# Performance work log

Measured on AMD Instinct MI355X. Metric: run time of the kernel, lower is better.

## Reference

```python
import jax, jax.numpy as jnp
import numpy as np

LN_EPS = 1e-5

def layer_norm(x, g, b):
    m = x.mean(-1, keepdims=True)
    v = ((x - m) ** 2).mean(-1, keepdims=True)
    return (x - m) / jnp.sqrt(v + LN_EPS) * g + b

def gat_conv(x, src, dst, W, att_src, att_dst, bias, heads, out_ch, concat):
    # PyG GATConv (eval mode, self-loops already included in src/dst).
    N = x.shape[0]
    h = (x @ W).reshape(N, heads, out_ch)                 # [N,H,C]
    a_src = (h * att_src).sum(-1)                          # [N,H]
    a_dst = (h * att_dst).sum(-1)                          # [N,H]
    e = jax.nn.leaky_relu(a_src[src] + a_dst[dst], 0.2)   # [E,H]
    emax = jax.ops.segment_max(e, dst, num_segments=N)    # [N,H]
    ee = jnp.exp(e - emax[dst])
    denom = jax.ops.segment_sum(ee, dst, num_segments=N)  # [N,H]
    alpha = ee / (denom[dst] + 1e-16)                      # [E,H]
    out = jax.ops.segment_sum(alpha[:, :, None] * h[src], dst, num_segments=N)  # [N,H,C]
    out = out.reshape(N, heads * out_ch) if concat else out.mean(axis=1)
    return out + bias

def setup_inputs() -> dict:
    key = jax.random.key(0)
    ks = jax.random.split(key, 32)
    N, G, E = 50000, 405, 300000
    RH, GH, H = 256, 256, 4
    def w(k, shape, fan_in):
        return jax.random.normal(k, shape, dtype=jnp.float32) * (1.0 / np.sqrt(fan_in))
    d = {}
    d["x"] = jax.random.normal(ks[0], (N, G), dtype=jnp.float32)
    d["edge_index"] = jax.random.randint(ks[1], (2, E), 0, N, dtype=jnp.int64)
    # JointEncoder
    d["enc_w1"] = w(ks[2], (G, RH), G); d["enc_b1"] = jnp.zeros(RH)
    d["ln1_g"] = jnp.ones(RH); d["ln1_b"] = jnp.zeros(RH)
    d["enc_w2"] = w(ks[3], (RH, RH), RH); d["enc_b2"] = jnp.zeros(RH)
    d["ln2_g"] = jnp.ones(RH); d["ln2_b"] = jnp.zeros(RH)
    d["w1"] = w(ks[4], (RH, H * GH), RH)
    d["att_src1"] = w(ks[5], (H, GH), GH); d["att_dst1"] = w(ks[6], (H, GH), GH)
    d["bias1"] = jnp.zeros(H * GH)
    d["res1_w"] = w(ks[7], (RH, H * GH), RH); d["res1_b"] = jnp.zeros(H * GH)
    d["w2"] = w(ks[8], (H * GH, 2 * 96), H * GH)
    d["att_src2"] = w(ks[9], (2, 96), 96); d["att_dst2"] = w(ks[10], (2, 96), 96)
    d["bias2"] = jnp.zeros(2 * 96)
    d["res2_w"] = w(ks[11], (H * GH, 2 * 96), H * GH); d["res2_b"] = jnp.zeros(2 * 96)
    d["w3"] = w(ks[12], (192, 128), 192)
    d["att_src3"] = w(ks[13], (1, 128), 128); d["att_dst3"] = w(ks[14], (1, 128), 128)
    d["bias3"] = jnp.zeros(128)
    d["res3_w"] = w(ks[15], (192, 128), 192); d["res3_b"] = jnp.zeros(128)
    # MLP head
    d["mlp_w1"] = w(ks[16], (128, 64), 128); d["mlp_b1"] = jnp.zeros(64)
    d["mlp_w2"] = w(ks[17], (64, 2), 64); d["mlp_b2"] = jnp.zeros(2)
    return d

def reference(x, edge_index, enc_w1, enc_b1, ln1_g, ln1_b, enc_w2, enc_b2, ln2_g, ln2_b,
              w1, att_src1, att_dst1, bias1, res1_w, res1_b,
              w2, att_src2, att_dst2, bias2, res2_w, res2_b,
              w3, att_src3, att_dst3, bias3, res3_w, res3_b,
              mlp_w1, mlp_b1, mlp_w2, mlp_b2):
    N = x.shape[0]
    loop = jnp.arange(N, dtype=edge_index.dtype)
    src = jnp.concatenate([edge_index[0], loop])
    dst = jnp.concatenate([edge_index[1], loop])
    # JointEncoder (eval: dropout is identity)
    h = jax.nn.relu(layer_norm(x @ enc_w1 + enc_b1, ln1_g, ln1_b))
    h = jax.nn.relu(layer_norm(h @ enc_w2 + enc_b2, ln2_g, ln2_b))
    # Block 1
    idn = h
    h = jax.nn.elu(gat_conv(h, src, dst, w1, att_src1, att_dst1, bias1, 4, 256, True))
    h = h + (idn @ res1_w + res1_b)
    # Block 2
    idn = h
    h = jax.nn.elu(gat_conv(h, src, dst, w2, att_src2, att_dst2, bias2, 2, 96, True))
    h = h + (idn @ res2_w + res2_b)
    # Block 3
    idn = h
    h = jax.nn.elu(gat_conv(h, src, dst, w3, att_src3, att_dst3, bias3, 1, 128, False))
    h = h + (idn @ res3_w + res3_b)
    # MLP head
    out = jax.nn.relu(h @ mlp_w1 + mlp_b1) @ mlp_w2 + mlp_b2
    return out
```

## Files before the change

kernel.cpp:

```cpp
#include <hip/hip_runtime.h>
#include <cstddef>

#define LN_EPS 1e-5f

typedef __bf16 bf16x8 __attribute__((ext_vector_type(8)));
typedef float  f32x4  __attribute__((ext_vector_type(4)));

typedef __attribute__((address_space(3))) unsigned int lds_u32;
typedef __attribute__((address_space(1))) unsigned int glb_u32;

__device__ __forceinline__ void gl2lds16(const void* g, void* l) {
    __builtin_amdgcn_global_load_lds((const glb_u32*)g, (lds_u32*)l, 16, 0, 0);
}

__device__ __forceinline__ float b2f(ushort h) {
    return __uint_as_float(((unsigned)h) << 16);
}
__device__ __forceinline__ ushort f2b(float f) {
    unsigned u = __float_as_uint(f);
    return (ushort)((u + 0x7fffu + ((u >> 16) & 1u)) >> 16);
}
__device__ __forceinline__ unsigned pack2(float lo, float hi) {
    return (unsigned)f2b(lo) | ((unsigned)f2b(hi) << 16);
}
__device__ __forceinline__ uint2 pack4(const f32x4 v) {
    return make_uint2(pack2(v[0], v[1]), pack2(v[2], v[3]));
}

__device__ __forceinline__ void xcd_map(int& bx, int& by) {
    int NX = gridDim.x, MBr = gridDim.y;
    int L = blockIdx.y * NX + blockIdx.x;
    int G = NX * 8;
    int g = L / G;
    if (g * 8 + 8 <= MBr) {
        int r = L - g * G;
        by = g * 8 + (r & 7);
        bx = r >> 3;
    } else {
        by = L / NX;
        bx = L - by * NX;
    }
}

__device__ __forceinline__ float wave_reduce_sum(float v) {
    #pragma unroll
    for (int off = 32; off > 0; off >>= 1) v += __shfl_down(v, off, 64);
    return v;
}
__device__ __forceinline__ float wave_allreduce_max(float v) {
    #pragma unroll
    for (int off = 32; off > 0; off >>= 1) v = fmaxf(v, __shfl_xor(v, off, 64));
    return v;
}
__device__ __forceinline__ float wave_allreduce_sum(float v) {
    #pragma unroll
    for (int off = 32; off > 0; off >>= 1) v += __shfl_xor(v, off, 64);
    return v;
}

__device__ __forceinline__ void stage32(const ushort* a0, const ushort* a1,
                                        const ushort* b0, const ushort* b1,
                                        ushort* __restrict__ As, ushort* __restrict__ Bs,
                                        int lb0, int lb1) {
    gl2lds16(a0, As + lb0);
    gl2lds16(a1, As + lb1);
    gl2lds16(b0, Bs + lb0);
    gl2lds16(b1, Bs + lb1);
}

__device__ __forceinline__ void mfma_loop32(const ushort* aA0, const ushort* aA1,
                                            const ushort* aB0, const ushort* aB1,
                                            ushort* __restrict__ As0, ushort* __restrict__ As1,
                                            ushort* __restrict__ Bs0, ushort* __restrict__ Bs1,
                                            int lb0, int lb1,
                                            int K, int wr, int wc, int cA, int l15,
                                            f32x4 acc[4][4]) {
    stage32(aA0, aA1, aB0, aB1, As0, Bs0, lb0, lb1);
    int p = 0;
    for (int k0 = 0; k0 < K; k0 += 32) {
        __syncthreads();
        const ushort* Ac = p ? As1 : As0;
        const ushort* Bc = p ? Bs1 : Bs0;
        ushort* Ad = p ? As0 : As1;
        ushort* Bd = p ? Bs0 : Bs1;
        int kn = k0 + 32;
        if (kn < K) stage32(aA0 + kn, aA1 + kn, aB0 + kn, aB1 + kn, Ad, Bd, lb0, lb1);
        bf16x8 af[4], bf[4];
        #pragma unroll
        for (int i = 0; i < 4; i++)
            af[i] = *reinterpret_cast<const bf16x8*>(&Ac[(wr + i * 16 + l15) * 32 + cA]);
        #pragma unroll
        for (int j = 0; j < 4; j++)
            bf[j] = *reinterpret_cast<const bf16x8*>(&Bc[(wc + j * 16 + l15) * 32 + cA]);
        #pragma unroll
        for (int i = 0; i < 4; i++)
            #pragma unroll
            for (int j = 0; j < 4; j++)
                acc[i][j] = __builtin_amdgcn_mfma_f32_16x16x32_bf16(bf[j], af[i], acc[i][j], 0, 0, 0);
        p ^= 1;
    }
    __syncthreads();
}

template<int EPI>
__global__ __launch_bounds__(256) void bgemm(const ushort* __restrict__ A,
                                             const ushort* __restrict__ BT,
                                             const float* __restrict__ bias,
                                             void* __restrict__ out, int ldc,
                                             float* __restrict__ Rf,
                                             float* __restrict__ Sf, int Fs,
                                             int M, int Ncols, int K, int lda) {
    __shared__ ushort As[2][128 * 32];
    __shared__ ushort Bs[2][128 * 32];
    const int tid = threadIdx.x;
    int bx, by; xcd_map(bx, by);
    const int m0 = by * 128, n0 = bx * 128;
    const int w = tid >> 6, lane = tid & 63;
    const int wr = (w >> 1) * 64, wc = (w & 1) * 64;
    const int quad = lane >> 4, l15 = lane & 15;
    const int cA = (quad ^ ((l15 >> 1) & 3)) * 8;
    const int lb0 = w * 512, lb1 = lb0 + 2048;

    const int s0 = tid, s1 = tid + 256;
    const int r0 = s0 >> 2, g0 = ((s0 & 3) ^ ((s0 >> 3) & 3)) * 8;
    const int r1 = s1 >> 2, g1 = ((s1 & 3) ^ ((s1 >> 3) & 3)) * 8;
    int ga0 = m0 + r0; if (ga0 >= M) ga0 = M - 1;
    int ga1 = m0 + r1; if (ga1 >= M) ga1 = M - 1;
    const ushort* aA0 = A + (size_t)ga0 * lda + g0;
    const ushort* aA1 = A + (size_t)ga1 * lda + g1;
    const ushort* aB0 = BT + (size_t)(n0 + r0) * K + g0;
    const ushort* aB1 = BT + (size_t)(n0 + r1) * K + g1;

    f32x4 acc[4][4] = {};
    mfma_loop32(aA0, aA1, aB0, aB1, As[0], As[1], Bs[0], Bs[1], lb0, lb1,
                K, wr, wc, cA, l15, acc);

    const int twoH = Ncols - 2 * Fs;
    #pragma unroll
    for (int i = 0; i < 4; i++) {
        int row = m0 + wr + i * 16 + l15;
        if (row >= M) continue;
        #pragma unroll
        for (int j = 0; j < 4; j++) {
            int colbase = n0 + wc + j * 16 + quad * 4;
            if (EPI == 0) {
                f32x4 v = acc[i][j];
                if (bias) {
                    float4 bv = *reinterpret_cast<const float4*>(&bias[colbase]);
                    v[0] += bv.x; v[1] += bv.y; v[2] += bv.z; v[3] += bv.w;
                }
                *reinterpret_cast<f32x4*>(&((float*)out)[(size_t)row * ldc + colbase]) = v;
            } else if (EPI == 3) {
                if (colbase >= Ncols) continue;
                float4 bv = *reinterpret_cast<const float4*>(&bias[colbase]);
                f32x4 v = acc[i][j];
                v[0] = fmaxf(v[0] + bv.x, 0.f); v[1] = fmaxf(v[1] + bv.y, 0.f);
                v[2] = fmaxf(v[2] + bv.z, 0.f); v[3] = fmaxf(v[3] + bv.w, 0.f);
                *reinterpret_cast<uint2*>(&((ushort*)out)[(size_t)row * ldc + colbase]) = pack4(v);
            } else {
                if (colbase + 3 < Fs) {
                    *reinterpret_cast<uint2*>(&((ushort*)out)[(size_t)row * Fs + colbase]) = pack4(acc[i][j]);
                } else if (colbase >= Fs && colbase + 3 < 2 * Fs) {
                    *reinterpret_cast<f32x4*>(&Rf[(size_t)row * Fs + (colbase - Fs)]) = acc[i][j];
                } else {
                    #pragma unroll
                    for (int r = 0; r < 4; r++) {
                        int col = colbase + r;
                        if (col < 2 * Fs || col >= Ncols) continue;
                        Sf[(size_t)row * twoH + (col - 2 * Fs)] = acc[i][j][r];
                    }
                }
            }
        }
    }
}

__global__ __launch_bounds__(256) void bgemm_b1(const ushort* __restrict__ accb,
                                                const ushort* __restrict__ w1T,
                                                const ushort* __restrict__ h1b,
                                                const ushort* __restrict__ res1T,
                                                const float* __restrict__ bias1,
                                                const float* __restrict__ res1b,
                                                ushort* __restrict__ H2b, int M) {
    __shared__ ushort As[2][128 * 32];
    __shared__ ushort Bs[2][128 * 32];
    const int tid = threadIdx.x;
    int bx, by; xcd_map(bx, by);
    const int m0 = by * 128, n0 = bx * 128;
    const int h = n0 >> 8;
    const int w = tid >> 6, lane = tid & 63;
    const int wr = (w >> 1) * 64, wc = (w & 1) * 64;
    const int quad = lane >> 4, l15 = lane & 15;
    const int cA = (quad ^ ((l15 >> 1) & 3)) * 8;
    const int lb0 = w * 512, lb1 = lb0 + 2048;

    const int s0 = tid, s1 = tid + 256;
    const int r0 = s0 >> 2, g0 = ((s0 & 3) ^ ((s0 >> 3) & 3)) * 8;
    const int r1 = s1 >> 2, g1 = ((s1 & 3) ^ ((s1 >> 3) & 3)) * 8;
    int ga0 = m0 + r0; if (ga0 >= M) ga0 = M - 1;
    int ga1 = m0 + r1; if (ga1 >= M) ga1 = M - 1;

    f32x4 acc[4][4] = {};

    mfma_loop32(accb + (size_t)ga0 * 1024 + h * 256 + g0,
                accb + (size_t)ga1 * 1024 + h * 256 + g1,
                w1T + (size_t)(n0 + r0) * 256 + g0,
                w1T + (size_t)(n0 + r1) * 256 + g1,
                As[0], As[1], Bs[0], Bs[1], lb0, lb1, 256, wr, wc, cA, l15, acc);

    #pragma unroll
    for (int i = 0; i < 4; i++) {
        #pragma unroll
        for (int j = 0; j < 4; j++) {
            int colbase = n0 + wc + j * 16 + quad * 4;
            float4 bv = *reinterpret_cast<const float4*>(&bias1[colbase]);
            float4 rv = *reinterpret_cast<const float4*>(&res1b[colbase]);
            float bb[4] = { bv.x, bv.y, bv.z, bv.w };
            float rr[4] = { rv.x, rv.y, rv.z, rv.w };
            #pragma unroll
            for (int r = 0; r < 4; r++) {
                float t = acc[i][j][r] + bb[r];
                t = t > 0.f ? t : (__expf(t) - 1.f);
                acc[i][j][r] = t + rr[r];
            }
        }
    }

    mfma_loop32(h1b + (size_t)ga0 * 256 + g0,
                h1b + (size_t)ga1 * 256 + g1,
                res1T + (size_t)(n0 + r0) * 256 + g0,
                res1T + (size_t)(n0 + r1) * 256 + g1,
                As[0], As[1], Bs[0], Bs[1], lb0, lb1, 256, wr, wc, cA, l15, acc);

    #pragma unroll
    for (int i = 0; i < 4; i++) {
        int row = m0 + wr + i * 16 + l15;
        if (row >= M) continue;
        #pragma unroll
        for (int j = 0; j < 4; j++) {
            int colbase = n0 + wc + j * 16 + quad * 4;
            *reinterpret_cast<uint2*>(&H2b[(size_t)row * 1024 + colbase]) = pack4(acc[i][j]);
        }
    }
}

__global__ void conv_pad_x_kernel(const float* __restrict__ x, ushort* __restrict__ xb, int N) {
    int t = blockIdx.x * 256 + threadIdx.x;
    if (t >= N * 448) return;
    int n = t / 448, k = t - n * 448;
    xb[t] = f2b(k < 405 ? x[(size_t)n * 405 + k] : 0.f);
}

__device__ __forceinline__ void prep_seg(int t, const float* src, ushort* dst,
                                         int K, int Nreal, int Kpad, int ldsrc) {
    int n = t / Kpad, k = t - n * Kpad;
    float v = (k < K && n < Nreal) ? src[(size_t)k * ldsrc + n] : 0.f;
    dst[t] = f2b(v);
}

__global__ void prep_all_kernel(const float* __restrict__ enc_w1, const float* __restrict__ enc_w2,
                                const float* __restrict__ w1, const float* __restrict__ res1_w,
                                const float* __restrict__ w2, const float* __restrict__ res2_w,
                                const float* __restrict__ w3, const float* __restrict__ res3_w,
                                const float* __restrict__ mlp_w1,
                                ushort* __restrict__ enc_w1T, ushort* __restrict__ enc_w2T,
                                ushort* __restrict__ w1T, ushort* __restrict__ res1T,
                                ushort* __restrict__ Bcat2T, ushort* __restrict__ Bcat3T,
                                ushort* __restrict__ mlpw1T) {
    int t = blockIdx.x * 256 + threadIdx.x;
    const int c0 = 114688;
    const int c1 = c0 + 65536;
    const int c2 = c1 + 262144;
    const int c3 = c2 + 262144;
    const int c4 = c3 + 196608;
    const int c5 = c4 + 196608;
    const int c6 = c5 + 126976;
    const int c7 = c6 + 24576;
    const int c8 = c7 + 24576;
    const int c9 = c8 + 24192;
    const int c10 = c9 + 16384;
    if (t < c0)      prep_seg(t,        enc_w1, enc_w1T, 405, 256, 448, 256);
    else if (t < c1) prep_seg(t - c0,   enc_w2, enc_w2T, 256, 256, 256, 256);
    else if (t < c2) prep_seg(t - c1,   w1,     w1T,     256, 1024, 256, 1024);
    else if (t < c3) prep_seg(t - c2,   res1_w, res1T,   256, 1024, 256, 1024);
    else if (t < c4) prep_seg(t - c3,   w2,     Bcat2T,  1024, 192, 1024, 192);
    else if (t < c5) prep_seg(t - c4,   res2_w, Bcat2T + (size_t)192 * 1024, 1024, 192, 1024, 192);
    else if (t < c6) Bcat2T[(size_t)388 * 1024 + (t - c5)] = 0;
    else if (t < c7) prep_seg(t - c6,   w3,     Bcat3T,  192, 128, 192, 128);
    else if (t < c8) prep_seg(t - c7,   res3_w, Bcat3T + (size_t)128 * 192, 192, 128, 192, 128);
    else if (t < c9) Bcat3T[(size_t)258 * 192 + (t - c8)] = 0;
    else if (t < c10) prep_seg(t - c9,  mlp_w1, mlpw1T,  128, 64, 128, 64);
}

__global__ __launch_bounds__(256) void ln_relu_kernel(const float* __restrict__ x,
                                                      const float* __restrict__ g,
                                                      const float* __restrict__ b,
                                                      ushort* __restrict__ out) {
    const int C = 256;
    int row = blockIdx.x;
    int tid = threadIdx.x;
    int lane = tid & 63, wid = tid >> 6;
    __shared__ float red[4];
    float v = x[(size_t)row * C + tid];
    float s = wave_reduce_sum(v);
    if (lane == 0) red[wid] = s;
    __syncthreads();
    float m = (red[0] + red[1] + red[2] + red[3]) * (1.f / C);
    __syncthreads();
    float d = v - m;
    float s2 = wave_reduce_sum(d * d);
    if (lane == 0) red[wid] = s2;
    __syncthreads();
    float var = (red[0] + red[1] + red[2] + red[3]) * (1.f / C);
    float rs = rsqrtf(var + LN_EPS);
    float o = d * rs * g[tid] + b[tid];
    out[(size_t)row * C + tid] = f2b(fmaxf(o, 0.f));
}

__global__ void fold_att_kernel(const float* __restrict__ W,
                                const float* __restrict__ att_s,
                                const float* __restrict__ att_d,
                                float* __restrict__ qs, float* __restrict__ qd,
                                int Cin, int Cout, int H) {
    int t = blockIdx.x * blockDim.x + threadIdx.x;
    if (t >= H * Cin) return;
    int h = t / Cin, k = t - h * Cin;
    const float* wrow = W + (size_t)k * (H * Cout) + (size_t)h * Cout;
    const float* as = att_s + (size_t)h * Cout;
    const float* ad = att_d + (size_t)h * Cout;
    float ss = 0.f, sd = 0.f;
    for (int c = 0; c < Cout; c++) { float wv = wrow[c]; ss += wv * as[c]; sd += wv * ad[c]; }
    qs[t] = ss;
    qd[t] = sd;
}

__global__ void fold_att_b16_kernel(const float* __restrict__ W,
                                    const float* __restrict__ att_s,
                                    const float* __restrict__ att_d,
                                    ushort* __restrict__ qs_b, ushort* __restrict__ qd_b,
                                    int Cin, int Cout, int H) {
    int t = blockIdx.x * blockDim.x + threadIdx.x;
    if (t >= H * Cin) return;
    int h = t / Cin, k = t - h * Cin;
    const float* wrow = W + (size_t)k * (H * Cout) + (size_t)h * Cout;
    const float* as = att_s + (size_t)h * Cout;
    const float* ad = att_d + (size_t)h * Cout;
    float ss = 0.f, sd = 0.f;
    for (int c = 0; c < Cout; c++) { float wv = wrow[c]; ss += wv * as[c]; sd += wv * ad[c]; }
    qs_b[t] = f2b(ss);
    qd_b[t] = f2b(sd);
}

__global__ __launch_bounds__(64) void att_scores4_kernel(const ushort* __restrict__ x,
                                                         const float* __restrict__ qs,
                                                         const float* __restrict__ qd,
                                                         float* __restrict__ a_s,
                                                         float* __restrict__ a_d) {
    int n = blockIdx.x;
    int lane = threadIdx.x;
    const ushort* xp = x + (size_t)n * 256 + lane * 4;
    uint2 xv = *reinterpret_cast<const uint2*>(xp);
    float v[4] = { b2f((ushort)(xv.x & 0xffff)), b2f((ushort)(xv.x >> 16)),
                   b2f((ushort)(xv.y & 0xffff)), b2f((ushort)(xv.y >> 16)) };
    float rs[4], rd[4];
    #pragma unroll
    for (int h = 0; h < 4; h++) {
        const float* qsp = qs + h * 256 + lane * 4;
        const float* qdp = qd + h * 256 + lane * 4;
        float ss = 0.f, sd = 0.f;
        #pragma unroll
        for (int k = 0; k < 4; k++) { ss += v[k] * qsp[k]; sd += v[k] * qdp[k]; }
        rs[h] = wave_reduce_sum(ss);
        rd[h] = wave_reduce_sum(sd);
    }
    if (lane == 0) {
        *reinterpret_cast<float4*>(&a_s[(size_t)n * 4]) = make_float4(rs[0], rs[1], rs[2], rs[3]);
        *reinterpret_cast<float4*>(&a_d[(size_t)n * 4]) = make_float4(rd[0], rd[1], rd[2], rd[3]);
    }
}

__device__ __forceinline__ void edge_sd(const int* ei, int e, int E, int& s, int& d) {
    if (e < E) { s = ei[e]; d = ei[E + e]; } else { s = d = e - E; }
}

__global__ void deg_kernel(const int* __restrict__ ei, int* __restrict__ deg, int E, int Et) {
    int e = blockIdx.x * blockDim.x + threadIdx.x;
    if (e >= Et) return;
    int s, d; edge_sd(ei, e, E, s, d);
    atomicAdd(&deg[d], 1);
}

__global__ __launch_bounds__(256) void scan1_kernel(const int* __restrict__ deg,
                                                    int* __restrict__ incl,
                                                    int* __restrict__ part, int N) {
    __shared__ int sd[256];
    int t = threadIdx.x;
    int i = blockIdx.x * 256 + t;
    int v = (i < N) ? deg[i] : 0;
    sd[t] = v; __syncthreads();
    #pragma unroll
    for (int o = 1; o < 256; o <<= 1) {
        int x = (t >= o) ? sd[t - o] : 0;
        __syncthreads();
        sd[t] += x;
        __syncthreads();
    }
    if (i < N) incl[i] = sd[t];
    if (t == 255) part[blockIdx.x] = sd[255];
}

__global__ __launch_bounds__(256) void scan2_kernel(int* __restrict__ part, int nb) {
    __shared__ int sd[256];
    int t = threadIdx.x;
    int v = (t < nb) ? part[t] : 0;
    sd[t] = v; __syncthreads();
    #pragma unroll
    for (int o = 1; o < 256; o <<= 1) {
        int x = (t >= o) ? sd[t - o] : 0;
        __syncthreads();
        sd[t] += x;
        __syncthreads();
    }
    if (t < nb) part[t] = sd[t];
}

__global__ void scan3_kernel(const int* __restrict__ incl, const int* __restrict__ deg,
                             const int* __restrict__ part, int* __restrict__ row_ptr, int N) {
    int i = blockIdx.x * blockDim.x + threadIdx.x;
    if (i >= N) return;
    int off = (blockIdx.x > 0) ? part[blockIdx.x - 1] : 0;
    row_ptr[i] = incl[i] - deg[i] + off;
}

__global__ void fill_kernel(const int* __restrict__ ei, const int* __restrict__ row_ptr,
                            int* __restrict__ cur, int* __restrict__ csr_src, int E, int Et) {
    int e = blockIdx.x * blockDim.x + threadIdx.x;
    if (e >= Et) return;
    int s, d; edge_sd(ei, e, E, s, d);
    int pos = row_ptr[d] + atomicAdd(&cur[d], 1);
    csr_src[pos] = s;
}

template<int H>
__global__ __launch_bounds__(64) void stats_kernel(const int* __restrict__ row_ptr,
                                                   const int* __restrict__ deg,
                                                   const int* __restrict__ csr_src,
                                                   const float* __restrict__ a_s, int sA,
                                                   const float* __restrict__ a_d, int sD,
                                                   float* __restrict__ alpha) {
    int d = blockIdx.x;
    int lane = threadIdx.x;
    int base = row_ptr[d], dg = deg[d];
    float ad[H];
    #pragma unroll
    for (int h = 0; h < H; h++) ad[h] = a_d[(size_t)d * sD + h];

    float mx[H];
    #pragma unroll
    for (int h = 0; h < H; h++) mx[h] = -1e30f;
    for (int j = lane; j < dg; j += 64) {
        int s = csr_src[base + j];
        #pragma unroll
        for (int h = 0; h < H; h++) {
            float sc = a_s[(size_t)s * sA + h] + ad[h];
            sc = sc > 0.f ? sc : 0.2f * sc;
            mx[h] = fmaxf(mx[h], sc);
        }
    }
    #pragma unroll
    for (int h = 0; h < H; h++) mx[h] = wave_allreduce_max(mx[h]);

    float sm[H];
    #pragma unroll
    for (int h = 0; h < H; h++) sm[h] = 0.f;
    for (int j = lane; j < dg; j += 64) {
        int s = csr_src[base + j];
        #pragma unroll
        for (int h = 0; h < H; h++) {
            float sc = a_s[(size_t)s * sA + h] + ad[h];
            sc = sc > 0.f ? sc : 0.2f * sc;
            sm[h] += __expf(sc - mx[h]);
        }
    }
    float rd[H];
    #pragma unroll
    for (int h = 0; h < H; h++) {
        sm[h] = wave_allreduce_sum(sm[h]);
        rd[h] = 1.f / (sm[h] + 1e-16f);
    }

    for (int j = lane; j < dg; j += 64) {
        int s = csr_src[base + j];
        #pragma unroll
        for (int h = 0; h < H; h++) {
            float sc = a_s[(size_t)s * sA + h] + ad[h];
            sc = sc > 0.f ? sc : 0.2f * sc;
            alpha[(size_t)(base + j) * H + h] = __expf(sc - mx[h]) * rd[h];
        }
    }
}

__global__ __launch_bounds__(128) void aggr_b1_all_kernel(const int* __restrict__ row_ptr,
                                                          const int* __restrict__ deg,
                                                          const int* __restrict__ csr_src,
                                                          const float* __restrict__ alpha,
                                                          const ushort* __restrict__ h1b,
                                                          ushort* __restrict__ accb) {
    int d = blockIdx.x;
    int t = threadIdx.x;
    int base = row_ptr[d], dg = deg[d];
    float a00 = 0, a01 = 0, a10 = 0, a11 = 0, a20 = 0, a21 = 0, a30 = 0, a31 = 0;
    for (int j = 0; j < dg; j++) {
        int s = csr_src[base + j];
        float4 a = *reinterpret_cast<const float4*>(&alpha[(size_t)(base + j) * 4]);
        unsigned v = reinterpret_cast<const unsigned*>(h1b + (size_t)s * 256)[t];
        float lo = b2f((ushort)(v & 0xffff)), hi = b2f((ushort)(v >> 16));
        a00 += a.x * lo; a01 += a.x * hi;
        a10 += a.y * lo; a11 += a.y * hi;
        a20 += a.z * lo; a21 += a.z * hi;
        a30 += a.w * lo; a31 += a.w * hi;
    }
    unsigned* o = reinterpret_cast<unsigned*>(accb + (size_t)d * 1024);
    o[t]       = pack2(a00, a01);
    o[t + 128] = pack2(a10, a11);
    o[t + 256] = pack2(a20, a21);
    o[t + 384] = pack2(a30, a31);
}

template<int H, int C, int F>
__global__ void aggr_comb_kernel(const int* __restrict__ row_ptr,
                                 const int* __restrict__ deg,
                                 const int* __restrict__ csr_src,
                                 const float* __restrict__ alpha,
                                 const ushort* __restrict__ g,
                                 const float* __restrict__ Rf,
                                 const float* __restrict__ gb,
                                 const float* __restrict__ rb,
                                 ushort* __restrict__ outb) {
    int d = blockIdx.x;
    int t = threadIdx.x;
    int hd = (2 * t) / C;
    int base = row_ptr[d], dg = deg[d];
    float lo = 0.f, hi = 0.f;
    for (int j = 0; j < dg; j++) {
        int s = csr_src[base + j];
        float a = alpha[(size_t)(base + j) * H + hd];
        unsigned v = reinterpret_cast<const unsigned*>(g + (size_t)s * F)[t];
        lo += a * b2f((ushort)(v & 0xffff));
        hi += a * b2f((ushort)(v >> 16));
    }
    int c0 = 2 * t, c1 = 2 * t + 1;
    float o0 = lo + gb[c0]; o0 = o0 > 0.f ? o0 : (__expf(o0) - 1.f);
    float o1 = hi + gb[c1]; o1 = o1 > 0.f ? o1 : (__expf(o1) - 1.f);
    o0 += Rf[(size_t)d * F + c0] + rb[c0];
    o1 += Rf[(size_t)d * F + c1] + rb[c1];
    reinterpret_cast<unsigned*>(outb)[(size_t)d * (F / 2) + t] = pack2(o0, o1);
}

__global__ __launch_bounds__(256) void mlp2_kernel(const ushort* __restrict__ A,
                                                   const float* __restrict__ W,
                                                   const float* __restrict__ b,
                                                   float* __restrict__ out, int M) {
    __shared__ float w[128];
    __shared__ float bb[2];
    int tid = threadIdx.x;
    if (tid < 128) w[tid] = W[tid];
    if (tid < 2) bb[tid] = b[tid];
    __syncthreads();
    int row = blockIdx.x * 256 + tid;
    if (row >= M) return;
    float a0 = bb[0], a1 = bb[1];
    const ushort* ap = A + (size_t)row * 64;
    #pragma unroll 8
    for (int k = 0; k < 64; k++) {
        float av = b2f(ap[k]);
        a0 += av * w[2 * k];
        a1 += av * w[2 * k + 1];
    }
    out[(size_t)row * 2] = a0;
    out[(size_t)row * 2 + 1] = a1;
}

extern "C" void kernel_launch(void* const* d_in, const int* in_sizes, int n_in,
                              void* d_out, int out_size, void* d_ws, size_t ws_size,
                              hipStream_t stream) {
    const float* x        = (const float*)d_in[0];
    const int*   ei       = (const int*)d_in[1];
    const float* enc_w1   = (const float*)d_in[2];
    const float* enc_b1   = (const float*)d_in[3];
    const float* ln1_g    = (const float*)d_in[4];
    const float* ln1_b    = (const float*)d_in[5];
    const float* enc_w2   = (const float*)d_in[6];
    const float* enc_b2   = (const float*)d_in[7];
    const float* ln2_g    = (const float*)d_in[8];
    const float* ln2_b    = (const float*)d_in[9];
    const float* w1       = (const float*)d_in[10];
    const float* att_src1 = (const float*)d_in[11];
    const float* att_dst1 = (const float*)d_in[12];
    const float* bias1    = (const float*)d_in[13];
    const float* res1_w   = (const float*)d_in[14];
    const float* res1_b   = (const float*)d_in[15];
    const float* w2       = (const float*)d_in[16];
    const float* att_src2 = (const float*)d_in[17];
    const float* att_dst2 = (const float*)d_in[18];
    const float* bias2    = (const float*)d_in[19];
    const float* res2_w   = (const float*)d_in[20];
    const float* res2_b   = (const float*)d_in[21];
    const float* w3       = (const float*)d_in[22];
    const float* att_src3 = (const float*)d_in[23];
    const float* att_dst3 = (const float*)d_in[24];
    const float* bias3    = (const float*)d_in[25];
    const float* res3_w   = (const float*)d_in[26];
    const float* res3_b   = (const float*)d_in[27];
    const float* mlp_w1   = (const float*)d_in[28];
    const float* mlp_b1   = (const float*)d_in[29];
    const float* mlp_w2   = (const float*)d_in[30];
    const float* mlp_b2   = (const float*)d_in[31];

    const int N  = in_sizes[0] / 405;
    const int E  = in_sizes[1] / 2;
    const int Et = E + N;
    const int NB = (N + 255) / 256;

    char* p = (char*)d_ws;
    char* R0 = p;
    char* R1 = R0 + (size_t)N * 896;
    char* R2 = R1 + (size_t)N * 512;
    char* R3 = R2 + (size_t)N * 512;
    char* R4 = R3 + (size_t)N * 2048;
    char* T  = R4 + (size_t)N * 2048;

    ushort* xb   = (ushort*)R0;
    ushort* H3b  = (ushort*)R0;
    ushort* M1b  = (ushort*)R0;
    ushort* h0b  = (ushort*)R1;
    ushort* G2b  = (ushort*)R1;
    ushort* h1b  = (ushort*)R2;
    ushort* G3b  = (ushort*)R2;
    ushort* H4b  = (ushort*)(R2 + (size_t)N * 256);
    float*  F1   = (float*)R3;
    ushort* H2b  = (ushort*)R3;
    ushort* accb = (ushort*)R4;
    float*  Rf   = (float*)R4;

    float* a_s   = (float*)T;                         T += (size_t)N * 4 * 4;
    float* a_d   = (float*)T;                         T += (size_t)N * 4 * 4;
    float* alpha = (float*)T;                         T += (size_t)Et * 4 * 4;
    float* qs    = (float*)T;                         T += 2048 * 4;
    float* qd    = (float*)T;                         T += 2048 * 4;
    int* deg     = (int*)T;                           T += (size_t)N * 4;
    int* cur     = (int*)T;                           T += (size_t)N * 4;
    int* row_ptr = (int*)T;                           T += (size_t)N * 4;
    int* incl    = (int*)T;                           T += (size_t)N * 4;
    int* part    = (int*)T;                           T += 256 * 4;
    int* csr_src = (int*)T;                           T += (size_t)Et * 4;
    ushort* enc_w1T = (ushort*)T;                     T += (size_t)256 * 448 * 2;
    ushort* enc_w2T = (ushort*)T;                     T += (size_t)256 * 256 * 2;
    ushort* w1T     = (ushort*)T;                     T += (size_t)1024 * 256 * 2;
    ushort* res1T   = (ushort*)T;                     T += (size_t)1024 * 256 * 2;
    ushort* Bcat2T  = (ushort*)T;                     T += (size_t)512 * 1024 * 2;
    ushort* Bcat3T  = (ushort*)T;                     T += (size_t)384 * 192 * 2;
    ushort* mlpw1T  = (ushort*)T;                     T += (size_t)128 * 128 * 2;

    auto cdiv = [](int a, int b) { return (a + b - 1) / b; };
    const int MB = cdiv(N, 128);

    hipMemsetAsync(deg, 0, (size_t)N * 8, stream);
    deg_kernel<<<cdiv(Et, 256), 256, 0, stream>>>(ei, deg, E, Et);
    scan1_kernel<<<NB, 256, 0, stream>>>(deg, incl, part, N);
    scan2_kernel<<<1, 256, 0, stream>>>(part, NB);
    scan3_kernel<<<NB, 256, 0, stream>>>(incl, deg, part, row_ptr, N);
    fill_kernel<<<cdiv(Et, 256), 256, 0, stream>>>(ei, row_ptr, cur, csr_src, E, Et);

    prep_all_kernel<<<cdiv(1314432, 256), 256, 0, stream>>>(
        enc_w1, enc_w2, w1, res1_w, w2, res2_w, w3, res3_w, mlp_w1,
        enc_w1T, enc_w2T, w1T, res1T, Bcat2T, Bcat3T, mlpw1T);

    conv_pad_x_kernel<<<cdiv(N * 448, 256), 256, 0, stream>>>(x, xb, N);
    bgemm<0><<<dim3(2, MB), 256, 0, stream>>>(xb, enc_w1T, enc_b1, F1, 256, nullptr, nullptr, 0, N, 256, 448, 448);
    ln_relu_kernel<<<N, 256, 0, stream>>>(F1, ln1_g, ln1_b, h0b);
    bgemm<0><<<dim3(2, MB), 256, 0, stream>>>(h0b, enc_w2T, enc_b2, F1, 256, nullptr, nullptr, 0, N, 256, 256, 256);
    ln_relu_kernel<<<N, 256, 0, stream>>>(F1, ln2_g, ln2_b, h1b);

    {
        fold_att_kernel<<<cdiv(4 * 256, 256), 256, 0, stream>>>(w1, att_src1, att_dst1, qs, qd, 256, 256, 4);
        att_scores4_kernel<<<N, 64, 0, stream>>>(h1b, qs, qd, a_s, a_d);
        stats_kernel<4><<<N, 64, 0, stream>>>(row_ptr, deg, csr_src, a_s, 4, a_d, 4, alpha);
        aggr_b1_all_kernel<<<N, 128, 0, stream>>>(row_ptr, deg, csr_src, alpha, h1b, accb);
        bgemm_b1<<<dim3(8, MB), 256, 0, stream>>>(accb, w1T, h1b, res1T, bias1, res1_b, H2b, N);
    }

    {
        fold_att_b16_kernel<<<cdiv(2 * 1024, 256), 256, 0, stream>>>(w2, att_src2, att_dst2,
            Bcat2T + (size_t)384 * 1024, Bcat2T + (size_t)386 * 1024, 1024, 96, 2);
        bgemm<5><<<dim3(4, MB), 256, 0, stream>>>(H2b, Bcat2T, nullptr, G2b, 0, Rf, a_s, 192, N, 388, 1024, 1024);
        stats_kernel<2><<<N, 64, 0, stream>>>(row_ptr, deg, csr_src, a_s, 4, a_s + 2, 4, alpha);
        aggr_comb_kernel<2, 96, 192><<<N, 96, 0, stream>>>(row_ptr, deg, csr_src, alpha, G2b,
                                                           Rf, bias2, res2_b, H3b);
    }

    {
        fold_att_b16_kernel<<<1, 256, 0, stream>>>(w3, att_src3, att_dst3,
            Bcat3T + (size_t)256 * 192, Bcat3T + (size_t)257 * 192, 192, 128, 1);
        bgemm<5><<<dim3(3, MB), 256, 0, stream>>>(H3b, Bcat3T, nullptr, G3b, 0, Rf, a_s, 128, N, 258, 192, 192);
        stats_kernel<1><<<N, 64, 0, stream>>>(row_ptr, deg, csr_src, a_s, 2, a_s + 1, 2, alpha);
        aggr_comb_kernel<1, 128, 128><<<N, 64, 0, stream>>>(row_ptr, deg, csr_src, alpha, G3b,
                                                            Rf, bias3, res3_b, H4b);
    }

    bgemm<3><<<dim3(1, MB), 256, 0, stream>>>(H4b, mlpw1T, mlp_b1, M1b, 64, nullptr, nullptr, 0, N, 64, 128, 128);
    mlp2_kernel<<<cdiv(N, 256), 256, 0, stream>>>(M1b, mlp_w2, mlp_b2, (float*)d_out, N);
}
```

Baseline: 894.1 us.

## Fuse softmax stats into aggregation, triple-buffer GEMM, fold scores and MLP tail

The GEMM main loop moves from a double-buffered LDS pipeline to a triple-buffered one with explicit vmcnt waits, so global-to-LDS loads run two stages ahead. The per-node softmax statistics kernels are merged into the aggregation kernels, which keep unnormalised exponentials in LDS for up to 256 edges and recompute the rest, so the alpha array is never written to or read from global memory. The attention score dot products for layer 1 are computed inside the second LayerNorm kernel, and the final 64-to-2 MLP layer is folded into the epilogue of the preceding GEMM. Together these cut kernel launches and intermediate memory traffic, at the cost of more LDS per block and recomputation for high-degree nodes.

```diff
diff --git a/kernel.cpp b/kernel.cpp
--- a/kernel.cpp
+++ b/kernel.cpp
@@ -70,21 +70,29 @@
 
 __device__ __forceinline__ void mfma_loop32(const ushort* aA0, const ushort* aA1,
                                             const ushort* aB0, const ushort* aB1,
-                                            ushort* __restrict__ As0, ushort* __restrict__ As1,
-                                            ushort* __restrict__ Bs0, ushort* __restrict__ Bs1,
+                                            ushort* __restrict__ As, ushort* __restrict__ Bs,
                                             int lb0, int lb1,
                                             int K, int wr, int wc, int cA, int l15,
                                             f32x4 acc[4][4]) {
-    stage32(aA0, aA1, aB0, aB1, As0, Bs0, lb0, lb1);
-    int p = 0;
-    for (int k0 = 0; k0 < K; k0 += 32) {
-        __syncthreads();
-        const ushort* Ac = p ? As1 : As0;
-        const ushort* Bc = p ? Bs1 : Bs0;
-        ushort* Ad = p ? As0 : As1;
-        ushort* Bd = p ? Bs0 : Bs1;
-        int kn = k0 + 32;
-        if (kn < K) stage32(aA0 + kn, aA1 + kn, aB0 + kn, aB1 + kn, Ad, Bd, lb0, lb1);
+    const int BUF = 128 * 32;
+    const int nk = K >> 5;
+    stage32(aA0, aA1, aB0, aB1, As, Bs, lb0, lb1);
+    if (nk > 1) stage32(aA0 + 32, aA1 + 32, aB0 + 32, aB1 + 32,
+                        As + BUF, Bs + BUF, lb0, lb1);
+    int cur = 0;
+    for (int t = 0; t < nk; t++) {
+        if (t + 1 < nk) asm volatile("s_waitcnt vmcnt(4)" ::: "memory");
+        else            asm volatile("s_waitcnt vmcnt(0)" ::: "memory");
+        __builtin_amdgcn_s_barrier();
+        __builtin_amdgcn_sched_barrier(0);
+        int kn = (t + 2) * 32;
+        if (kn < K) {
+            int nb = cur + 2; if (nb >= 3) nb -= 3;
+            stage32(aA0 + kn, aA1 + kn, aB0 + kn, aB1 + kn,
+                    As + nb * BUF, Bs + nb * BUF, lb0, lb1);
+        }
+        const ushort* Ac = As + cur * BUF;
+        const ushort* Bc = Bs + cur * BUF;
         bf16x8 af[4], bf[4];
         #pragma unroll
         for (int i = 0; i < 4; i++)
@@ -97,7 +105,7 @@
             #pragma unroll
             for (int j = 0; j < 4; j++)
                 acc[i][j] = __builtin_amdgcn_mfma_f32_16x16x32_bf16(bf[j], af[i], acc[i][j], 0, 0, 0);
-        p ^= 1;
+        cur++; if (cur >= 3) cur -= 3;
     }
     __syncthreads();
 }
@@ -110,8 +118,8 @@
                                              float* __restrict__ Rf,
                                              float* __restrict__ Sf, int Fs,
                                              int M, int Ncols, int K, int lda) {
-    __shared__ ushort As[2][128 * 32];
-    __shared__ ushort Bs[2][128 * 32];
+    __shared__ ushort As[3][128 * 32];
+    __shared__ ushort Bs[3][128 * 32];
     const int tid = threadIdx.x;
     int bx, by; xcd_map(bx, by);
     const int m0 = by * 128, n0 = bx * 128;
@@ -132,8 +140,38 @@
     const ushort* aB1 = BT + (size_t)(n0 + r1) * K + g1;
 
     f32x4 acc[4][4] = {};
-    mfma_loop32(aA0, aA1, aB0, aB1, As[0], As[1], Bs[0], Bs[1], lb0, lb1,
+    mfma_loop32(aA0, aA1, aB0, aB1, As[0], Bs[0], lb0, lb1,
                 K, wr, wc, cA, l15, acc);
+
+    if (EPI == 4) {
+        if (wc == 0) {
+            #pragma unroll
+            for (int i = 0; i < 4; i++) {
+                float o0 = 0.f, o1 = 0.f;
+                #pragma unroll
+                for (int j = 0; j < 4; j++) {
+                    int colbase = j * 16 + quad * 4;
+                    float4 bv = *reinterpret_cast<const float4*>(&bias[colbase]);
+                    float bb[4] = { bv.x, bv.y, bv.z, bv.w };
+                    #pragma unroll
+                    for (int r = 0; r < 4; r++) {
+                        float vv = fmaxf(acc[i][j][r] + bb[r], 0.f);
+                        int c = colbase + r;
+                        o0 += vv * Rf[2 * c];
+                        o1 += vv * Rf[2 * c + 1];
+                    }
+                }
+                o0 += __shfl_xor(o0, 16, 64); o0 += __shfl_xor(o0, 32, 64);
+                o1 += __shfl_xor(o1, 16, 64); o1 += __shfl_xor(o1, 32, 64);
+                int row = m0 + wr + i * 16 + l15;
+                if (quad == 0 && row < M) {
+                    ((float*)out)[(size_t)row * 2]     = o0 + Sf[0];
+                    ((float*)out)[(size_t)row * 2 + 1] = o1 + Sf[1];
+                }
+            }
+        }
+        return;
+    }
 
     const int twoH = Ncols - 2 * Fs;
     #pragma unroll
@@ -150,14 +188,7 @@
                     v[0] += bv.x; v[1] += bv.y; v[2] += bv.z; v[3] += bv.w;
                 }
                 *reinterpret_cast<f32x4*>(&((float*)out)[(size_t)row * ldc + colbase]) = v;
-            } else if (EPI == 3) {
-                if (colbase >= Ncols) continue;
-                float4 bv = *reinterpret_cast<const float4*>(&bias[colbase]);
-                f32x4 v = acc[i][j];
-                v[0] = fmaxf(v[0] + bv.x, 0.f); v[1] = fmaxf(v[1] + bv.y, 0.f);
-                v[2] = fmaxf(v[2] + bv.z, 0.f); v[3] = fmaxf(v[3] + bv.w, 0.f);
-                *reinterpret_cast<uint2*>(&((ushort*)out)[(size_t)row * ldc + colbase]) = pack4(v);
-            } else {
+            } else if (EPI == 5) {
                 if (colbase + 3 < Fs) {
                     *reinterpret_cast<uint2*>(&((ushort*)out)[(size_t)row * Fs + colbase]) = pack4(acc[i][j]);
                 } else if (colbase >= Fs && colbase + 3 < 2 * Fs) {
@@ -182,8 +213,8 @@
                                                 const float* __restrict__ bias1,
                                                 const float* __restrict__ res1b,
                                                 ushort* __restrict__ H2b, int M) {
-    __shared__ ushort As[2][128 * 32];
-    __shared__ ushort Bs[2][128 * 32];
+    __shared__ ushort As[3][128 * 32];
+    __shared__ ushort Bs[3][128 * 32];
     const int tid = threadIdx.x;
     int bx, by; xcd_map(bx, by);
     const int m0 = by * 128, n0 = bx * 128;
@@ -206,7 +237,7 @@
                 accb + (size_t)ga1 * 1024 + h * 256 + g1,
                 w1T + (size_t)(n0 + r0) * 256 + g0,
                 w1T + (size_t)(n0 + r1) * 256 + g1,
-                As[0], As[1], Bs[0], Bs[1], lb0, lb1, 256, wr, wc, cA, l15, acc);
+                As[0], Bs[0], lb0, lb1, 256, wr, wc, cA, l15, acc);
 
     #pragma unroll
     for (int i = 0; i < 4; i++) {
@@ -230,7 +261,7 @@
                 h1b + (size_t)ga1 * 256 + g1,
                 res1T + (size_t)(n0 + r0) * 256 + g0,
                 res1T + (size_t)(n0 + r1) * 256 + g1,
-                As[0], As[1], Bs[0], Bs[1], lb0, lb1, 256, wr, wc, cA, l15, acc);
+                As[0], Bs[0], lb0, lb1, 256, wr, wc, cA, l15, acc);
 
     #pragma unroll
     for (int i = 0; i < 4; i++) {
@@ -292,15 +323,21 @@
     else if (t < c10) prep_seg(t - c9,  mlp_w1, mlpw1T,  128, 64, 128, 64);
 }
 
-__global__ __launch_bounds__(256) void ln_relu_kernel(const float* __restrict__ x,
-                                                      const float* __restrict__ g,
-                                                      const float* __restrict__ b,
-                                                      ushort* __restrict__ out) {
+template<int H>
+__global__ __launch_bounds__(256) void ln_relu_score_kernel(const float* __restrict__ x,
+                                                            const float* __restrict__ g,
+                                                            const float* __restrict__ b,
+                                                            const float* __restrict__ qs,
+                                                            const float* __restrict__ qd,
+                                                            ushort* __restrict__ out,
+                                                            float* __restrict__ a_s,
+                                                            float* __restrict__ a_d) {
     const int C = 256;
     int row = blockIdx.x;
     int tid = threadIdx.x;
     int lane = tid & 63, wid = tid >> 6;
     __shared__ float red[4];
+    __shared__ float sred[8][4];
     float v = x[(size_t)row * C + tid];
     float s = wave_reduce_sum(v);
     if (lane == 0) red[wid] = s;
@@ -313,8 +350,22 @@
     __syncthreads();
     float var = (red[0] + red[1] + red[2] + red[3]) * (1.f / C);
     float rs = rsqrtf(var + LN_EPS);
-    float o = d * rs * g[tid] + b[tid];
-    out[(size_t)row * C + tid] = f2b(fmaxf(o, 0.f));
+    float o = fmaxf(d * rs * g[tid] + b[tid], 0.f);
+    out[(size_t)row * C + tid] = f2b(o);
+    if (H > 0) {
+        #pragma unroll
+        for (int hh = 0; hh < H; hh++) {
+            float ss = wave_reduce_sum(o * qs[hh * 256 + tid]);
+            float sd = wave_reduce_sum(o * qd[hh * 256 + tid]);
+            if (lane == 0) { sred[hh][wid] = ss; sred[H + hh][wid] = sd; }
+        }
+        __syncthreads();
+        if (tid < 2 * H) {
+            float t = sred[tid][0] + sred[tid][1] + sred[tid][2] + sred[tid][3];
+            if (tid < H) a_s[(size_t)row * H + tid] = t;
+            else         a_d[(size_t)row * H + (tid - H)] = t;
+        }
+    }
 }
 
 __global__ void fold_att_kernel(const float* __restrict__ W,
@@ -351,34 +402,6 @@
     qd_b[t] = f2b(sd);
 }
 
-__global__ __launch_bounds__(64) void att_scores4_kernel(const ushort* __restrict__ x,
-                                                         const float* __restrict__ qs,
-                                                         const float* __restrict__ qd,
-                                                         float* __restrict__ a_s,
-                                                         float* __restrict__ a_d) {
-    int n = blockIdx.x;
-    int lane = threadIdx.x;
-    const ushort* xp = x + (size_t)n * 256 + lane * 4;
-    uint2 xv = *reinterpret_cast<const uint2*>(xp);
-    float v[4] = { b2f((ushort)(xv.x & 0xffff)), b2f((ushort)(xv.x >> 16)),
-                   b2f((ushort)(xv.y & 0xffff)), b2f((ushort)(xv.y >> 16)) };
-    float rs[4], rd[4];
-    #pragma unroll
-    for (int h = 0; h < 4; h++) {
-        const float* qsp = qs + h * 256 + lane * 4;
-        const float* qdp = qd + h * 256 + lane * 4;
-        float ss = 0.f, sd = 0.f;
-        #pragma unroll
-        for (int k = 0; k < 4; k++) { ss += v[k] * qsp[k]; sd += v[k] * qdp[k]; }
-        rs[h] = wave_reduce_sum(ss);
-        rd[h] = wave_reduce_sum(sd);
-    }
-    if (lane == 0) {
-        *reinterpret_cast<float4*>(&a_s[(size_t)n * 4]) = make_float4(rs[0], rs[1], rs[2], rs[3]);
-        *reinterpret_cast<float4*>(&a_d[(size_t)n * 4]) = make_float4(rd[0], rd[1], rd[2], rd[3]);
-    }
-}
-
 __device__ __forceinline__ void edge_sd(const int* ei, int e, int E, int& s, int& d) {
     if (e < E) { s = ei[e]; d = ei[E + e]; } else { s = d = e - E; }
 }
@@ -441,84 +464,72 @@
     csr_src[pos] = s;
 }
 
-template<int H>
-__global__ __launch_bounds__(64) void stats_kernel(const int* __restrict__ row_ptr,
-                                                   const int* __restrict__ deg,
-                                                   const int* __restrict__ csr_src,
-                                                   const float* __restrict__ a_s, int sA,
-                                                   const float* __restrict__ a_d, int sD,
-                                                   float* __restrict__ alpha) {
-    int d = blockIdx.x;
-    int lane = threadIdx.x;
+#define ACAP 256
+
+__global__ __launch_bounds__(128) void aggr_b1_fused_kernel(const int* __restrict__ row_ptr,
+                                                            const int* __restrict__ deg,
+                                                            const int* __restrict__ csr_src,
+                                                            const float* __restrict__ a_s,
+                                                            const float* __restrict__ a_d,
+                                                            const ushort* __restrict__ h1b,
+                                                            ushort* __restrict__ accb) {
+    __shared__ float alf[ACAP][4];
+    __shared__ float sstat[8];
+    int d = blockIdx.x, t = threadIdx.x;
     int base = row_ptr[d], dg = deg[d];
-    float ad[H];
-    #pragma unroll
-    for (int h = 0; h < H; h++) ad[h] = a_d[(size_t)d * sD + h];
-
-    float mx[H];
-    #pragma unroll
-    for (int h = 0; h < H; h++) mx[h] = -1e30f;
-    for (int j = lane; j < dg; j += 64) {
-        int s = csr_src[base + j];
-        #pragma unroll
-        for (int h = 0; h < H; h++) {
-            float sc = a_s[(size_t)s * sA + h] + ad[h];
-            sc = sc > 0.f ? sc : 0.2f * sc;
-            mx[h] = fmaxf(mx[h], sc);
-        }
-    }
-    #pragma unroll
-    for (int h = 0; h < H; h++) mx[h] = wave_allreduce_max(mx[h]);
-
-    float sm[H];
-    #pragma unroll
-    for (int h = 0; h < H; h++) sm[h] = 0.f;
-    for (int j = lane; j < dg; j += 64) {
-        int s = csr_src[base + j];
-        #pragma unroll
-        for (int h = 0; h < H; h++) {
-            float sc = a_s[(size_t)s * sA + h] + ad[h];
-            sc = sc > 0.f ? sc : 0.2f * sc;
-            sm[h] += __expf(sc - mx[h]);
-        }
-    }
-    float rd[H];
-    #pragma unroll
-    for (int h = 0; h < H; h++) {
-        sm[h] = wave_allreduce_sum(sm[h]);
-        rd[h] = 1.f / (sm[h] + 1e-16f);
-    }
-
-    for (int j = lane; j < dg; j += 64) {
-        int s = csr_src[base + j];
-        #pragma unroll
-        for (int h = 0; h < H; h++) {
-            float sc = a_s[(size_t)s * sA + h] + ad[h];
-            sc = sc > 0.f ? sc : 0.2f * sc;
-            alpha[(size_t)(base + j) * H + h] = __expf(sc - mx[h]) * rd[h];
-        }
-    }
-}
-
-__global__ __launch_bounds__(128) void aggr_b1_all_kernel(const int* __restrict__ row_ptr,
-                                                          const int* __restrict__ deg,
-                                                          const int* __restrict__ csr_src,
-                                                          const float* __restrict__ alpha,
-                                                          const ushort* __restrict__ h1b,
-                                                          ushort* __restrict__ accb) {
-    int d = blockIdx.x;
-    int t = threadIdx.x;
-    int base = row_ptr[d], dg = deg[d];
+    float4 ad = *reinterpret_cast<const float4*>(&a_d[(size_t)d * 4]);
+    if (t < 64) {
+        float m0 = -1e30f, m1 = -1e30f, m2 = -1e30f, m3 = -1e30f;
+        for (int j = t; j < dg; j += 64) {
+            int s = csr_src[base + j];
+            float4 sv = *reinterpret_cast<const float4*>(&a_s[(size_t)s * 4]);
+            float c0 = sv.x + ad.x; c0 = c0 > 0.f ? c0 : 0.2f * c0; m0 = fmaxf(m0, c0);
+            float c1 = sv.y + ad.y; c1 = c1 > 0.f ? c1 : 0.2f * c1; m1 = fmaxf(m1, c1);
+            float c2 = sv.z + ad.z; c2 = c2 > 0.f ? c2 : 0.2f * c2; m2 = fmaxf(m2, c2);
+            float c3 = sv.w + ad.w; c3 = c3 > 0.f ? c3 : 0.2f * c3; m3 = fmaxf(m3, c3);
+        }
+        m0 = wave_allreduce_max(m0); m1 = wave_allreduce_max(m1);
+        m2 = wave_allreduce_max(m2); m3 = wave_allreduce_max(m3);
+        float s0 = 0.f, s1 = 0.f, s2 = 0.f, s3 = 0.f;
+        for (int j = t; j < dg; j += 64) {
+            int s = csr_src[base + j];
+            float4 sv = *reinterpret_cast<const float4*>(&a_s[(size_t)s * 4]);
+            float c0 = sv.x + ad.x; c0 = c0 > 0.f ? c0 : 0.2f * c0; float e0 = __expf(c0 - m0); s0 += e0;
+            float c1 = sv.y + ad.y; c1 = c1 > 0.f ? c1 : 0.2f * c1; float e1 = __expf(c1 - m1); s1 += e1;
+            float c2 = sv.z + ad.z; c2 = c2 > 0.f ? c2 : 0.2f * c2; float e2 = __expf(c2 - m2); s2 += e2;
+            float c3 = sv.w + ad.w; c3 = c3 > 0.f ? c3 : 0.2f * c3; float e3 = __expf(c3 - m3); s3 += e3;
+            if (j < ACAP) { alf[j][0] = e0; alf[j][1] = e1; alf[j][2] = e2; alf[j][3] = e3; }
+        }
+        s0 = wave_allreduce_sum(s0); s1 = wave_allreduce_sum(s1);
+        s2 = wave_allreduce_sum(s2); s3 = wave_allreduce_sum(s3);
+        if (t == 0) {
+            sstat[0] = m0; sstat[1] = m1; sstat[2] = m2; sstat[3] = m3;
+            sstat[4] = 1.f / (s0 + 1e-16f); sstat[5] = 1.f / (s1 + 1e-16f);
+            sstat[6] = 1.f / (s2 + 1e-16f); sstat[7] = 1.f / (s3 + 1e-16f);
+        }
+    }
+    __syncthreads();
+    float r0 = sstat[4], r1 = sstat[5], r2 = sstat[6], r3 = sstat[7];
     float a00 = 0, a01 = 0, a10 = 0, a11 = 0, a20 = 0, a21 = 0, a30 = 0, a31 = 0;
     for (int j = 0; j < dg; j++) {
         int s = csr_src[base + j];
-        float4 a = *reinterpret_cast<const float4*>(&alpha[(size_t)(base + j) * 4]);
+        float al0, al1, al2, al3;
+        if (j < ACAP) {
+            al0 = alf[j][0] * r0; al1 = alf[j][1] * r1;
+            al2 = alf[j][2] * r2; al3 = alf[j][3] * r3;
+        } else {
+            float4 sv = *reinterpret_cast<const float4*>(&a_s[(size_t)s * 4]);
+            float c0 = sv.x + ad.x; c0 = c0 > 0.f ? c0 : 0.2f * c0; al0 = __expf(c0 - sstat[0]) * r0;
+            float c1 = sv.y + ad.y; c1 = c1 > 0.f ? c1 : 0.2f * c1; al1 = __expf(c1 - sstat[1]) * r1;
+            float c2 = sv.z + ad.z; c2 = c2 > 0.f ? c2 : 0.2f * c2; al2 = __expf(c2 - sstat[2]) * r2;
+            float c3 = sv.w + ad.w; c3 = c3 > 0.f ? c3 : 0.2f * c3; al3 = __expf(c3 - sstat[3]) * r3;
+        }
         unsigned v = reinterpret_cast<const unsigned*>(h1b + (size_t)s * 256)[t];
         float lo = b2f((ushort)(v & 0xffff)), hi = b2f((ushort)(v >> 16));
-        a00 += a.x * lo; a01 += a.x * hi;
-        a10 += a.y * lo; a11 += a.y * hi;
-        a20 += a.z * lo; a21 += a.z * hi;
-        a30 += a.w * lo; a31 += a.w * hi;
+        a00 += al0 * lo; a01 += al0 * hi;
+        a10 += al1 * lo; a11 += al1 * hi;
+        a20 += al2 * lo; a21 += al2 * hi;
+        a30 += al3 * lo; a31 += al3 * hi;
     }
     unsigned* o = reinterpret_cast<unsigned*>(accb + (size_t)d * 1024);
     o[t]       = pack2(a00, a01);
@@ -527,27 +538,74 @@
     o[t + 384] = pack2(a30, a31);
 }
 
-template<int H, int C, int F>
-__global__ void aggr_comb_kernel(const int* __restrict__ row_ptr,
-                                 const int* __restrict__ deg,
-                                 const int* __restrict__ csr_src,
-                                 const float* __restrict__ alpha,
-                                 const ushort* __restrict__ g,
-                                 const float* __restrict__ Rf,
-                                 const float* __restrict__ gb,
-                                 const float* __restrict__ rb,
-                                 ushort* __restrict__ outb) {
+template<int H, int C, int F, int NT>
+__global__ __launch_bounds__(NT) void aggr_comb_fused_kernel(const int* __restrict__ row_ptr,
+                                                             const int* __restrict__ deg,
+                                                             const int* __restrict__ csr_src,
+                                                             const float* __restrict__ as,
+                                                             const ushort* __restrict__ g,
+                                                             const float* __restrict__ Rf,
+                                                             const float* __restrict__ gb,
+                                                             const float* __restrict__ rb,
+                                                             ushort* __restrict__ outb) {
+    __shared__ float alf[ACAP][H];
+    __shared__ float sstat[2 * H];
     int d = blockIdx.x;
     int t = threadIdx.x;
+    int base = row_ptr[d], dg = deg[d];
+    if (t < 64) {
+        float ad[H], mx[H];
+        #pragma unroll
+        for (int h = 0; h < H; h++) { ad[h] = as[(size_t)d * 2 * H + H + h]; mx[h] = -1e30f; }
+        for (int j = t; j < dg; j += 64) {
+            int s = csr_src[base + j];
+            #pragma unroll
+            for (int h = 0; h < H; h++) {
+                float c = as[(size_t)s * 2 * H + h] + ad[h];
+                c = c > 0.f ? c : 0.2f * c;
+                mx[h] = fmaxf(mx[h], c);
+            }
+        }
+        #pragma unroll
+        for (int h = 0; h < H; h++) mx[h] = wave_allreduce_max(mx[h]);
+        float sm[H];
+        #pragma unroll
+        for (int h = 0; h < H; h++) sm[h] = 0.f;
+        for (int j = t; j < dg; j += 64) {
+            int s = csr_src[base + j];
+            #pragma unroll
+            for (int h = 0; h < H; h++) {
+                float c = as[(size_t)s * 2 * H + h] + ad[h];
+                c = c > 0.f ? c : 0.2f * c;
+                float e = __expf(c - mx[h]);
+                sm[h] += e;
+                if (j < ACAP) alf[j][h] = e;
+            }
+        }
+        #pragma unroll
+        for (int h = 0; h < H; h++) sm[h] = wave_allreduce_sum(sm[h]);
+        if (t == 0) {
+            #pragma unroll
+            for (int h = 0; h < H; h++) { sstat[h] = mx[h]; sstat[H + h] = 1.f / (sm[h] + 1e-16f); }
+        }
+    }
+    __syncthreads();
     int hd = (2 * t) / C;
-    int base = row_ptr[d], dg = deg[d];
+    float mxv = sstat[hd], rdv = sstat[H + hd];
+    float adv = as[(size_t)d * 2 * H + H + hd];
     float lo = 0.f, hi = 0.f;
     for (int j = 0; j < dg; j++) {
         int s = csr_src[base + j];
-        float a = alpha[(size_t)(base + j) * H + hd];
+        float al;
+        if (j < ACAP) al = alf[j][hd] * rdv;
+        else {
+            float c = as[(size_t)s * 2 * H + hd] + adv;
+            c = c > 0.f ? c : 0.2f * c;
+            al = __expf(c - mxv) * rdv;
+        }
         unsigned v = reinterpret_cast<const unsigned*>(g + (size_t)s * F)[t];
-        lo += a * b2f((ushort)(v & 0xffff));
-        hi += a * b2f((ushort)(v >> 16));
+        lo += al * b2f((ushort)(v & 0xffff));
+        hi += al * b2f((ushort)(v >> 16));
     }
     int c0 = 2 * t, c1 = 2 * t + 1;
     float o0 = lo + gb[c0]; o0 = o0 > 0.f ? o0 : (__expf(o0) - 1.f);
@@ -555,30 +613,6 @@
     o0 += Rf[(size_t)d * F + c0] + rb[c0];
     o1 += Rf[(size_t)d * F + c1] + rb[c1];
     reinterpret_cast<unsigned*>(outb)[(size_t)d * (F / 2) + t] = pack2(o0, o1);
-}
-
-__global__ __launch_bounds__(256) void mlp2_kernel(const ushort* __restrict__ A,
-                                                   const float* __restrict__ W,
-                                                   const float* __restrict__ b,
-                                                   float* __restrict__ out, int M) {
-    __shared__ float w[128];
-    __shared__ float bb[2];
-    int tid = threadIdx.x;
-    if (tid < 128) w[tid] = W[tid];
-    if (tid < 2) bb[tid] = b[tid];
-    __syncthreads();
-    int row = blockIdx.x * 256 + tid;
-    if (row >= M) return;
-    float a0 = bb[0], a1 = bb[1];
-    const ushort* ap = A + (size_t)row * 64;
-    #pragma unroll 8
-    for (int k = 0; k < 64; k++) {
-        float av = b2f(ap[k]);
-        a0 += av * w[2 * k];
-        a1 += av * w[2 * k + 1];
-    }
-    out[(size_t)row * 2] = a0;
-    out[(size_t)row * 2 + 1] = a1;
 }
 
 extern "C" void kernel_launch(void* const* d_in, const int* in_sizes, int n_in,
@@ -632,7 +666,6 @@
 
     ushort* xb   = (ushort*)R0;
     ushort* H3b  = (ushort*)R0;
-    ushort* M1b  = (ushort*)R0;
     ushort* h0b  = (ushort*)R1;
     ushort* G2b  = (ushort*)R1;
     ushort* h1b  = (ushort*)R2;
@@ -645,7 +678,6 @@
 
     float* a_s   = (float*)T;                         T += (size_t)N * 4 * 4;
     float* a_d   = (float*)T;                         T += (size_t)N * 4 * 4;
-    float* alpha = (float*)T;                         T += (size_t)Et * 4 * 4;
     float* qs    = (float*)T;                         T += 2048 * 4;
     float* qd    = (float*)T;                         T += 2048 * 4;
     int* deg     = (int*)T;                           T += (size_t)N * 4;
@@ -676,38 +708,33 @@
         enc_w1, enc_w2, w1, res1_w, w2, res2_w, w3, res3_w, mlp_w1,
         enc_w1T, enc_w2T, w1T, res1T, Bcat2T, Bcat3T, mlpw1T);
 
+    fold_att_kernel<<<cdiv(4 * 256, 256), 256, 0, stream>>>(w1, att_src1, att_dst1, qs, qd, 256, 256, 4);
+
     conv_pad_x_kernel<<<cdiv(N * 448, 256), 256, 0, stream>>>(x, xb, N);
     bgemm<0><<<dim3(2, MB), 256, 0, stream>>>(xb, enc_w1T, enc_b1, F1, 256, nullptr, nullptr, 0, N, 256, 448, 448);
-    ln_relu_kernel<<<N, 256, 0, stream>>>(F1, ln1_g, ln1_b, h0b);
+    ln_relu_score_kernel<0><<<N, 256, 0, stream>>>(F1, ln1_g, ln1_b, nullptr, nullptr, h0b, nullptr, nullptr);
     bgemm<0><<<dim3(2, MB), 256, 0, stream>>>(h0b, enc_w2T, enc_b2, F1, 256, nullptr, nullptr, 0, N, 256, 256, 256);
-    ln_relu_kernel<<<N, 256, 0, stream>>>(F1, ln2_g, ln2_b, h1b);
-
-    {
-        fold_att_kernel<<<cdiv(4 * 256, 256), 256, 0, stream>>>(w1, att_src1, att_dst1, qs, qd, 256, 256, 4);
-        att_scores4_kernel<<<N, 64, 0, stream>>>(h1b, qs, qd, a_s, a_d);
-        stats_kernel<4><<<N, 64, 0, stream>>>(row_ptr, deg, csr_src, a_s, 4, a_d, 4, alpha);
-        aggr_b1_all_kernel<<<N, 128, 0, stream>>>(row_ptr, deg, csr_src, alpha, h1b, accb);
-        bgemm_b1<<<dim3(8, MB), 256, 0, stream>>>(accb, w1T, h1b, res1T, bias1, res1_b, H2b, N);
-    }
+    ln_relu_score_kernel<4><<<N, 256, 0, stream>>>(F1, ln2_g, ln2_b, qs, qd, h1b, a_s, a_d);
+
+    aggr_b1_fused_kernel<<<N, 128, 0, stream>>>(row_ptr, deg, csr_src, a_s, a_d, h1b, accb);
+    bgemm_b1<<<dim3(8, MB), 256, 0, stream>>>(accb, w1T, h1b, res1T, bias1, res1_b, H2b, N);
 
     {
         fold_att_b16_kernel<<<cdiv(2 * 1024, 256), 256, 0, stream>>>(w2, att_src2, att_dst2,
             Bcat2T + (size_t)384 * 1024, Bcat2T + (size_t)386 * 1024, 1024, 96, 2);
         bgemm<5><<<dim3(4, MB), 256, 0, stream>>>(H2b, Bcat2T, nullptr, G2b, 0, Rf, a_s, 192, N, 388, 1024, 1024);
-        stats_kernel<2><<<N, 64, 0, stream>>>(row_ptr, deg, csr_src, a_s, 4, a_s + 2, 4, alpha);
-        aggr_comb_kernel<2, 96, 192><<<N, 96, 0, stream>>>(row_ptr, deg, csr_src, alpha, G2b,
-                                                           Rf, bias2, res2_b, H3b);
+        aggr_comb_fused_kernel<2, 96, 192, 96><<<N, 96, 0, stream>>>(row_ptr, deg, csr_src, a_s,
+                                                                     G2b, Rf, bias2, res2_b, H3b);
     }
 
     {
         fold_att_b16_kernel<<<1, 256, 0, stream>>>(w3, att_src3, att_dst3,
             Bcat3T + (size_t)256 * 192, Bcat3T + (size_t)257 * 192, 192, 128, 1);
         bgemm<5><<<dim3(3, MB), 256, 0, stream>>>(H3b, Bcat3T, nullptr, G3b, 0, Rf, a_s, 128, N, 258, 192, 192);
-        stats_kernel<1><<<N, 64, 0, stream>>>(row_ptr, deg, csr_src, a_s, 2, a_s + 1, 2, alpha);
-        aggr_comb_kernel<1, 128, 128><<<N, 64, 0, stream>>>(row_ptr, deg, csr_src, alpha, G3b,
-                                                            Rf, bias3, res3_b, H4b);
-    }
-
-    bgemm<3><<<dim3(1, MB), 256, 0, stream>>>(H4b, mlpw1T, mlp_b1, M1b, 64, nullptr, nullptr, 0, N, 64, 128, 128);
-    mlp2_kernel<<<cdiv(N, 256), 256, 0, stream>>>(M1b, mlp_w2, mlp_b2, (float*)d_out, N);
-}
+        aggr_comb_fused_kernel<1, 128, 128, 64><<<N, 64, 0, stream>>>(row_ptr, deg, csr_src, a_s,
+                                                                      G3b, Rf, bias3, res3_b, H4b);
+    }
+
+    bgemm<4><<<dim3(1, MB), 256, 0, stream>>>(H4b, mlpw1T, mlp_b1, d_out, 2,
+                                              (float*)mlp_w2, (float*)mlp_b2, 0, N, 64, 128, 128);
+}
```

New measurement: 922.2 us. 1.03x slower.
